# Kernel tuning notes

Measured on AMD Instinct MI355X. Metric: run time of the kernel, lower is better.

Reference implementation:

```python
import jax, jax.numpy as jnp
import numpy as np
from jax import lax


def setup_inputs() -> dict:
    key = jax.random.key(0)
    ks = jax.random.split(key, 6)
    B, S, C, HID, H, K = 8, 2048, 768, 768, 12, 9
    return {
        "query": jax.random.normal(ks[0], (B, S, C), jnp.float32),
        "value": jax.random.normal(ks[1], (B, S, C), jnp.float32),
        "hidden_states": jax.random.normal(ks[2], (B, S, HID), jnp.float32),
        "dw_weight": jax.random.normal(ks[3], (HID, 1, K), jnp.float32) * (2.0 / K) ** 0.5,
        "pw_weight": jax.random.normal(ks[4], (C, HID, 1), jnp.float32) * (2.0 / HID) ** 0.5,
        "sep_bias": jnp.zeros((C,), jnp.float32),
        "attn_W": jax.random.normal(ks[5], (H * K, C), jnp.float32) * (1.0 / C) ** 0.5,
        "attn_b": jnp.zeros((H * K,), jnp.float32),
        "num_heads": H,
        "kernel_size": K,
    }


def reference(query, value, hidden_states, dw_weight, pw_weight, sep_bias,
              attn_W, attn_b, num_heads, kernel_size):
    K = kernel_size
    H = num_heads
    B, S, C = value.shape  # all_head_size = C
    D = C // H             # attention_head_size
    HID = hidden_states.shape[-1]
    pad = K // 2

    # --- SeparableConv1d: depthwise (groups=HID) then pointwise 1x1 ---
    x = jnp.transpose(hidden_states, (0, 2, 1))  # [B, HID, S]
    dn = ("NCH", "OIH", "NCH")
    dw = lax.conv_general_dilated(x, dw_weight, window_strides=(1,),
                                  padding=[(pad, pad)], dimension_numbers=dn,
                                  feature_group_count=HID)  # [B, HID, S]
    pw = lax.conv_general_dilated(dw, pw_weight, window_strides=(1,),
                                  padding=[(0, 0)], dimension_numbers=dn)  # [B, C, S]
    ks_out = jnp.transpose(pw, (0, 2, 1)) + sep_bias  # [B, S, C]

    # --- dynamic conv kernel: gated projection + (double) softmax ---
    conv_attn = ks_out * query                                   # [B, S, C]
    filt = conv_attn @ attn_W.T + attn_b                          # [B, S, H*K]
    filt = filt.reshape(B, S, H, K)
    # original code applies softmax twice (once in SDConv, once in LightConv)
    filt = jax.nn.softmax(jax.nn.softmax(filt, axis=-1), axis=-1)

    # --- light conv: unfold value along seq and contract over window ---
    vpad = jnp.pad(value, ((0, 0), (pad, pad), (0, 0)))           # [B, S+K-1, C]
    unf = jnp.stack([vpad[:, k:k + S, :] for k in range(K)], axis=-1)  # [B,S,C,K]
    unf = unf.reshape(B, S, H, D, K)
    out = jnp.einsum("bshdk,bshk->bshd", unf, filt)               # [B,S,H,D]
    return out
```

## Files before the change

kernel.cpp:

```cpp
#include <hip/hip_runtime.h>
#include <hip/hip_bf16.h>
#include <stdint.h>

#define B_   8
#define S_   2048
#define C_   768
#define HID_ 768
#define H_   12
#define KW   9
#define D_   64
#define M_   (B_ * S_)
#define PADW 4
#define HK_  108
#define NPAD 128

typedef __attribute__((ext_vector_type(4))) float  floatx4;
typedef __attribute__((ext_vector_type(8))) __bf16 bf16x8;

#define GLD_LDS16(gptr, lptr)                                                  \
    __builtin_amdgcn_global_load_lds(                                          \
        (__attribute__((address_space(1))) void*)(gptr),                       \
        (__attribute__((address_space(3))) void*)(lptr), 16, 0, 0)

__global__ __launch_bounds__(256) void convert_w_kernel(
    const float* __restrict__ pwW, const float* __restrict__ attnW,
    __hip_bfloat16* __restrict__ pwWb, __hip_bfloat16* __restrict__ attnWb)
{
    int i = blockIdx.x * 256 + threadIdx.x;
    if (i < C_ * HID_) pwWb[i] = __float2bfloat16(pwW[i]);
    if (i < NPAD * HID_) {
        int n = i / HID_;
        float v = (n < HK_) ? attnW[i] : 0.0f;
        attnWb[i] = __float2bfloat16(v);
    }
}

#define TSD 16

__global__ __launch_bounds__(256) void dwconv_kernel(
    const float* __restrict__ hidden, const float* __restrict__ dw_w,
    __hip_bfloat16* __restrict__ dw_out)
{
    int idx  = blockIdx.x * 256 + threadIdx.x;
    int hq   = idx % (HID_ / 4);
    int rest = idx / (HID_ / 4);
    int sc   = rest % (S_ / TSD);
    int b    = rest / (S_ / TSD);
    int h    = hq * 4;
    int s0   = sc * TSD;
    size_t base = (size_t)b * S_ * HID_ + h;

    float w[36];
    const float4* wp = reinterpret_cast<const float4*>(dw_w + (size_t)h * KW);
#pragma unroll
    for (int i = 0; i < 9; ++i) {
        float4 t = wp[i];
        w[4 * i + 0] = t.x; w[4 * i + 1] = t.y;
        w[4 * i + 2] = t.z; w[4 * i + 3] = t.w;
    }

    float4 win[KW];
#pragma unroll
    for (int k = 0; k < 8; ++k) {
        int sp = s0 + k - PADW;
        float4 v = {0.f, 0.f, 0.f, 0.f};
        if ((unsigned)sp < (unsigned)S_)
            v = *reinterpret_cast<const float4*>(&hidden[base + (size_t)sp * HID_]);
        win[k] = v;
    }

#pragma unroll
    for (int i = 0; i < TSD; ++i) {
        int sp = s0 + i + PADW;
        float4 nv = {0.f, 0.f, 0.f, 0.f};
        if ((unsigned)sp < (unsigned)S_)
            nv = *reinterpret_cast<const float4*>(&hidden[base + (size_t)sp * HID_]);
        win[8] = nv;

        float a0 = 0.f, a1 = 0.f, a2 = 0.f, a3 = 0.f;
#pragma unroll
        for (int k = 0; k < KW; ++k) {
            a0 += win[k].x * w[k];
            a1 += win[k].y * w[9 + k];
            a2 += win[k].z * w[18 + k];
            a3 += win[k].w * w[27 + k];
        }
        union { __hip_bfloat16 bv[4]; uint2 u; } o;
        o.bv[0] = __float2bfloat16(a0);
        o.bv[1] = __float2bfloat16(a1);
        o.bv[2] = __float2bfloat16(a2);
        o.bv[3] = __float2bfloat16(a3);
        *reinterpret_cast<uint2*>(&dw_out[base + (size_t)(s0 + i) * HID_]) = o.u;

#pragma unroll
        for (int k = 0; k < 8; ++k) win[k] = win[k + 1];
    }
}

#define BKK 64

template <int MODE, int TBM>
__global__ __launch_bounds__(256) void gemm_bt_kernel(
    const __hip_bfloat16* __restrict__ A,
    const __hip_bfloat16* __restrict__ Bt,
    const float* __restrict__ bias,
    const float* __restrict__ query,
    __hip_bfloat16* __restrict__ outB,
    float* __restrict__ outF,
    int ntN)
{
    constexpr int MF = TBM / 32;
    __shared__ __align__(16) __hip_bfloat16 Alds[TBM * BKK];
    __shared__ __align__(16) __hip_bfloat16 Blds[64 * BKK];

    const int t    = threadIdx.x;
    const int lane = t & 63;
    const int wave = t >> 6;
    const int wr   = wave >> 1, wc = wave & 1;
    const int l16  = lane & 15, lq = lane >> 4;

    const int nwg  = (int)gridDim.x;
    const int chunk = nwg >> 3;
    const int wg   = ((int)blockIdx.x & 7) * chunk + ((int)blockIdx.x >> 3);

    const int tm   = wg / ntN;
    const int tn   = wg % ntN;
    const int row0 = tm * TBM;
    const int col0 = tn * 64;

    const int K = HID_;

    floatx4 acc[MF][2];
#pragma unroll
    for (int i = 0; i < MF; ++i)
#pragma unroll
        for (int j = 0; j < 2; ++j) acc[i][j] = (floatx4){0.f, 0.f, 0.f, 0.f};

    const int srow = t >> 3;
    const int scol = (t & 7) * 8;
    char* aBase = (char*)Alds + wave * 1024;
    char* bBase = (char*)Blds + wave * 1024;

    for (int kt = 0; kt < K; kt += BKK) {
#pragma unroll
        for (int i = 0; i < MF; ++i) {
            const __hip_bfloat16* ga = A + (size_t)(row0 + i * 32 + srow) * K + kt + scol;
            GLD_LDS16(const_cast<__hip_bfloat16*>(ga), aBase + i * 4096);
        }
#pragma unroll
        for (int i = 0; i < 2; ++i) {
            const __hip_bfloat16* gb = Bt + (size_t)(col0 + i * 32 + srow) * K + kt + scol;
            GLD_LDS16(const_cast<__hip_bfloat16*>(gb), bBase + i * 4096);
        }
        __syncthreads();

        const bf16x8* A8 = reinterpret_cast<const bf16x8*>(Alds);
        const bf16x8* B8 = reinterpret_cast<const bf16x8*>(Blds);
#pragma unroll
        for (int ks = 0; ks < 2; ++ks) {
            bf16x8 av[MF], bv[2];
#pragma unroll
            for (int m = 0; m < MF; ++m)
                av[m] = A8[(wr * (TBM / 2) + m * 16 + l16) * 8 + ks * 4 + lq];
#pragma unroll
            for (int n = 0; n < 2; ++n)
                bv[n] = B8[(wc * 32 + n * 16 + l16) * 8 + ks * 4 + lq];
#pragma unroll
            for (int m = 0; m < MF; ++m)
#pragma unroll
                for (int n = 0; n < 2; ++n)
                    acc[m][n] = __builtin_amdgcn_mfma_f32_16x16x32_bf16(
                        av[m], bv[n], acc[m][n], 0, 0, 0);
        }
        __syncthreads();
    }

    const int orow0 = row0 + wr * (TBM / 2);
    const int ocol0 = col0 + wc * 32;
#pragma unroll
    for (int m = 0; m < MF; ++m) {
#pragma unroll
        for (int n = 0; n < 2; ++n) {
            const int col = ocol0 + n * 16 + l16;
            if (MODE == 0) {
                const float bv = bias[col];
#pragma unroll
                for (int j = 0; j < 4; ++j) {
                    const int row = orow0 + m * 16 + lq * 4 + j;
                    float v = (acc[m][n][j] + bv) * query[(size_t)row * C_ + col];
                    outB[(size_t)row * C_ + col] = __float2bfloat16(v);
                }
            } else {
#pragma unroll
                for (int j = 0; j < 4; ++j) {
                    const int row = orow0 + m * 16 + lq * 4 + j;
                    outF[(size_t)row * NPAD + col] = acc[m][n][j];
                }
            }
        }
    }
}

__global__ __launch_bounds__(256) void softmax2_kernel(
    const float* __restrict__ logits, const float* __restrict__ attn_b,
    float* __restrict__ filt)
{
    int r = blockIdx.x * 256 + threadIdx.x;
    int h = r % H_;
    int m = r / H_;

    float v[KW];
#pragma unroll
    for (int k = 0; k < KW; ++k)
        v[k] = logits[(size_t)m * NPAD + h * KW + k] + attn_b[h * KW + k];

#pragma unroll
    for (int pass = 0; pass < 2; ++pass) {
        float mx = v[0];
#pragma unroll
        for (int k = 1; k < KW; ++k) mx = fmaxf(mx, v[k]);
        float s = 0.f;
#pragma unroll
        for (int k = 0; k < KW; ++k) { v[k] = __expf(v[k] - mx); s += v[k]; }
        float inv = 1.f / s;
#pragma unroll
        for (int k = 0; k < KW; ++k) v[k] *= inv;
    }
#pragma unroll
    for (int k = 0; k < KW; ++k) filt[(size_t)r * KW + k] = v[k];
}

#define TSL 16
#define SCHK 256

__global__ __launch_bounds__(256) void lightconv_kernel(
    const float* __restrict__ value, const float* __restrict__ filt,
    float* __restrict__ out)
{
    __shared__ float fl[SCHK * KW];

    const int tid = threadIdx.x;
    const int blk = blockIdx.x;
    const int nSC = S_ / SCHK;
    const int b   = blk / (H_ * nSC);
    const int rem = blk % (H_ * nSC);
    const int h   = rem / nSC;
    const int sch = rem % nSC;
    const int S0  = sch * SCHK;

    {
        const size_t r0 = ((size_t)b * S_ + S0) * H_ + h;
#pragma unroll
        for (int i = 0; i < 9; ++i) {
            int j  = tid + 256 * i;
            int so = j / KW;
            int k  = j - so * KW;
            fl[j] = filt[(r0 + (size_t)so * H_) * KW + k];
        }
    }
    __syncthreads();

    const int d4 = tid & 15;
    const int sg = tid >> 4;
    const int s0 = S0 + sg * TSL;
    const size_t vbase = (size_t)b * S_ * C_ + h * D_ + d4 * 4;
    const float* flrow = &fl[(sg * TSL) * KW];

    float4 win[KW];
#pragma unroll
    for (int k = 0; k < 8; ++k) {
        int sp = s0 + k - PADW;
        float4 v = {0.f, 0.f, 0.f, 0.f};
        if ((unsigned)sp < (unsigned)S_)
            v = *reinterpret_cast<const float4*>(&value[vbase + (size_t)sp * C_]);
        win[k] = v;
    }

#pragma unroll
    for (int i = 0; i < TSL; ++i) {
        int sp = s0 + i + PADW;
        float4 nv = {0.f, 0.f, 0.f, 0.f};
        if ((unsigned)sp < (unsigned)S_)
            nv = *reinterpret_cast<const float4*>(&value[vbase + (size_t)sp * C_]);
        win[8] = nv;

        float4 acc = {0.f, 0.f, 0.f, 0.f};
#pragma unroll
        for (int k = 0; k < KW; ++k) {
            float f = flrow[i * KW + k];
            acc.x += win[k].x * f;
            acc.y += win[k].y * f;
            acc.z += win[k].z * f;
            acc.w += win[k].w * f;
        }
        *reinterpret_cast<float4*>(&out[vbase + (size_t)(s0 + i) * C_]) = acc;

#pragma unroll
        for (int k = 0; k < 8; ++k) win[k] = win[k + 1];
    }
}

extern "C" void kernel_launch(void* const* d_in, const int* in_sizes, int n_in,
                              void* d_out, int out_size, void* d_ws, size_t ws_size,
                              hipStream_t stream)
{
    const float* query  = (const float*)d_in[0];
    const float* value  = (const float*)d_in[1];
    const float* hidden = (const float*)d_in[2];
    const float* dw_w   = (const float*)d_in[3];
    const float* pw_w   = (const float*)d_in[4];
    const float* sep_b  = (const float*)d_in[5];
    const float* attn_W = (const float*)d_in[6];
    const float* attn_b = (const float*)d_in[7];
    float* out = (float*)d_out;

    char* ws = (char*)d_ws;
    __hip_bfloat16* dwb    = (__hip_bfloat16*)(ws);
    __hip_bfloat16* cab    = (__hip_bfloat16*)(ws + 25165824);
    __hip_bfloat16* pwWb   = (__hip_bfloat16*)(ws + 50331648);
    __hip_bfloat16* attnWb = (__hip_bfloat16*)(ws + 51511296);
    float*          logits = (float*)(ws + 51707904);
    float*          filt   = (float*)(ws + 60096512);

    convert_w_kernel<<<(C_ * HID_) / 256, 256, 0, stream>>>(pw_w, attn_W, pwWb, attnWb);

    dwconv_kernel<<<(M_ * (HID_ / 4)) / (256 * TSD), 256, 0, stream>>>(hidden, dw_w, dwb);

    gemm_bt_kernel<0, 128><<<(M_ / 128) * (C_ / 64), 256, 0, stream>>>(
        dwb, pwWb, sep_b, query, cab, nullptr, C_ / 64);

    gemm_bt_kernel<1, 64><<<(M_ / 64) * (NPAD / 64), 256, 0, stream>>>(
        cab, attnWb, nullptr, nullptr, nullptr, logits, NPAD / 64);

    softmax2_kernel<<<(M_ * H_) / 256, 256, 0, stream>>>(logits, attn_b, filt);

    lightconv_kernel<<<B_ * H_ * (S_ / SCHK), 256, 0, stream>>>(value, filt, out);
}
```

Measured before the change: 106.6 us.

## Replace pointwise GEMM with 256x256 double-buffered 8-phase pipelined MFMA kernel

The pointwise-conv GEMM (16384x768x768) moves from a 128x64 tile kernel with a load-then-sync-then-compute loop to a 512-thread kernel with 256x256 tiles. It uses double-buffered LDS filled by global_load_lds, XOR-swizzled LDS addressing, and an 8-phase schedule that overlaps the next tile's loads with MFMA work on the current one. This is meant to raise data reuse, cut LDS bank conflicts and hide global memory latency. The cost is 128 KB of LDS per block and only 192 blocks, which may leave some compute units underused. It also relies on hand-placed vmcnt waits and barriers being correct.

```diff
diff --git a/kernel.cpp b/kernel.cpp
--- a/kernel.cpp
+++ b/kernel.cpp
@@ -22,6 +22,11 @@
         (__attribute__((address_space(1))) void*)(gptr),                       \
         (__attribute__((address_space(3))) void*)(lptr), 16, 0, 0)
 
+#define WAITVM4() do { asm volatile("s_waitcnt vmcnt(4)" ::: "memory"); \
+                       __builtin_amdgcn_sched_barrier(0); } while (0)
+#define WAITVM0() do { asm volatile("s_waitcnt vmcnt(0)" ::: "memory"); \
+                       __builtin_amdgcn_sched_barrier(0); } while (0)
+
 __global__ __launch_bounds__(256) void convert_w_kernel(
     const float* __restrict__ pwW, const float* __restrict__ attnW,
     __hip_bfloat16* __restrict__ pwWb, __hip_bfloat16* __restrict__ attnWb)
@@ -97,18 +102,143 @@
     }
 }
 
-#define BKK 64
-
-template <int MODE, int TBM>
-__global__ __launch_bounds__(256) void gemm_bt_kernel(
+__global__ __launch_bounds__(512, 2) void gemm1_8phase_kernel(
     const __hip_bfloat16* __restrict__ A,
     const __hip_bfloat16* __restrict__ Bt,
     const float* __restrict__ bias,
     const float* __restrict__ query,
-    __hip_bfloat16* __restrict__ outB,
+    __hip_bfloat16* __restrict__ outB)
+{
+    __shared__ __align__(16) __hip_bfloat16 Ash[2][2][128 * 64];
+    __shared__ __align__(16) __hip_bfloat16 Bsh[2][2][128 * 64];
+
+    const int t    = threadIdx.x;
+    const int lane = t & 63;
+    const int wave = t >> 6;
+    const int wr   = wave >> 2;
+    const int wc   = wave & 3;
+    const int l16  = lane & 15, lq = lane >> 4;
+
+    const int bid = (int)blockIdx.x;
+    const int wg  = (bid & 7) * 24 + (bid >> 3);
+    const int tm  = wg / 3, tn = wg % 3;
+    const int row0 = tm * 256, col0 = tn * 256;
+
+    const int srow    = wave * 8 + (lane >> 3);
+    const int srcslot = (lane & 7) ^ ((lane >> 3) & 7);
+    const __hip_bfloat16* aSrc = A  + (size_t)(row0 + srow) * HID_ + srcslot * 8;
+    const __hip_bfloat16* bSrc = Bt + (size_t)(col0 + srow) * HID_ + srcslot * 8;
+
+    floatx4 acc[2][2][4][2];
+#pragma unroll
+    for (int a = 0; a < 2; ++a)
+#pragma unroll
+    for (int b = 0; b < 2; ++b)
+#pragma unroll
+    for (int m = 0; m < 4; ++m)
+#pragma unroll
+    for (int n = 0; n < 2; ++n) acc[a][b][m][n] = (floatx4){0.f, 0.f, 0.f, 0.f};
+
+#define STG_A(tile, h) do {                                                    \
+    const __hip_bfloat16* _g = aSrc + (size_t)(h) * 128 * HID_ + (tile) * 64;  \
+    char* _l = (char*)(&Ash[(tile) & 1][h][0]) + wave * 1024;                  \
+    GLD_LDS16(_g, _l);                                                         \
+    GLD_LDS16(_g + 64 * HID_, _l + 8192);                                      \
+} while (0)
+
+#define STG_B(tile, h) do {                                                    \
+    const __hip_bfloat16* _g = bSrc + (size_t)(h) * 128 * HID_ + (tile) * 64;  \
+    char* _l = (char*)(&Bsh[(tile) & 1][h][0]) + wave * 1024;                  \
+    GLD_LDS16(_g, _l);                                                         \
+    GLD_LDS16(_g + 64 * HID_, _l + 8192);                                      \
+} while (0)
+
+#define PHASE(buf, mh, nh, STAGES, BOUNDARY) do {                              \
+    bf16x8 av[4][2], bv[2][2];                                                 \
+    const char* _ab = (const char*)(&Ash[buf][mh][0]);                         \
+    const char* _bb = (const char*)(&Bsh[buf][nh][0]);                         \
+    _Pragma("unroll") for (int _m = 0; _m < 4; ++_m) {                         \
+        const int _r = wr * 64 + _m * 16 + l16;                                \
+        _Pragma("unroll") for (int _k = 0; _k < 2; ++_k)                       \
+            av[_m][_k] = *(const bf16x8*)(_ab + _r * 128 +                     \
+                ((_k * 64 + lq * 16) ^ ((l16 & 7) << 4)));                     \
+    }                                                                          \
+    _Pragma("unroll") for (int _n = 0; _n < 2; ++_n) {                         \
+        const int _r = wc * 32 + _n * 16 + l16;                                \
+        _Pragma("unroll") for (int _k = 0; _k < 2; ++_k)                       \
+            bv[_n][_k] = *(const bf16x8*)(_bb + _r * 128 +                     \
+                ((_k * 64 + lq * 16) ^ ((l16 & 7) << 4)));                     \
+    }                                                                          \
+    STAGES;                                                                    \
+    __builtin_amdgcn_s_barrier();                                              \
+    asm volatile("s_waitcnt lgkmcnt(0)" ::: "memory");                         \
+    __builtin_amdgcn_sched_barrier(0);                                         \
+    __builtin_amdgcn_s_setprio(1);                                             \
+    _Pragma("unroll") for (int _m = 0; _m < 4; ++_m)                           \
+        _Pragma("unroll") for (int _n = 0; _n < 2; ++_n)                       \
+            _Pragma("unroll") for (int _k = 0; _k < 2; ++_k)                   \
+                acc[mh][nh][_m][_n] = __builtin_amdgcn_mfma_f32_16x16x32_bf16( \
+                    av[_m][_k], bv[_n][_k], acc[mh][nh][_m][_n], 0, 0, 0);     \
+    __builtin_amdgcn_s_setprio(0);                                             \
+    BOUNDARY;                                                                  \
+    __builtin_amdgcn_s_barrier();                                              \
+} while (0)
+
+    STG_A(0, 0);
+    STG_B(0, 1);
+    STG_B(0, 0);
+    STG_A(0, 1);
+    STG_A(1, 0);
+    STG_B(1, 1);
+    WAITVM4();
+    __builtin_amdgcn_s_barrier();
+
+    for (int it = 0; it < 6; ++it) {
+        const int t1 = 2 * it + 1, t2 = 2 * it + 2, t3 = 2 * it + 3;
+        const bool nl = (it < 5);
+        PHASE(0, 0, 0, { STG_B(t1, 0); }, {});
+        PHASE(0, 0, 1, { STG_A(t1, 1); }, {});
+        PHASE(0, 1, 1, { if (nl) STG_A(t2, 0); }, {});
+        PHASE(0, 1, 0, { if (nl) STG_B(t2, 1); },
+              { if (nl) { WAITVM4(); } else { WAITVM0(); } });
+        PHASE(1, 0, 0, { if (nl) STG_B(t2, 0); }, {});
+        PHASE(1, 0, 1, { if (nl) STG_A(t2, 1); }, {});
+        PHASE(1, 1, 1, { if (nl) STG_A(t3, 0); }, {});
+        PHASE(1, 1, 0, { if (nl) STG_B(t3, 1); }, { if (nl) WAITVM4(); });
+    }
+
+#pragma unroll
+    for (int mh = 0; mh < 2; ++mh)
+#pragma unroll
+    for (int nh = 0; nh < 2; ++nh)
+#pragma unroll
+    for (int n = 0; n < 2; ++n) {
+        const int col = col0 + nh * 128 + wc * 32 + n * 16 + l16;
+        const float bvv = bias[col];
+#pragma unroll
+        for (int m = 0; m < 4; ++m) {
+#pragma unroll
+            for (int j = 0; j < 4; ++j) {
+                const int row = row0 + mh * 128 + wr * 64 + m * 16 + lq * 4 + j;
+                float v = (acc[mh][nh][m][n][j] + bvv) * query[(size_t)row * C_ + col];
+                outB[(size_t)row * C_ + col] = __float2bfloat16(v);
+            }
+        }
+    }
+#undef STG_A
+#undef STG_B
+#undef PHASE
+}
+
+#define BKK 64
+
+__global__ __launch_bounds__(256) void gemm2_kernel(
+    const __hip_bfloat16* __restrict__ A,
+    const __hip_bfloat16* __restrict__ Bt,
     float* __restrict__ outF,
     int ntN)
 {
+    constexpr int TBM = 64;
     constexpr int MF = TBM / 32;
     __shared__ __align__(16) __hip_bfloat16 Alds[TBM * BKK];
     __shared__ __align__(16) __hip_bfloat16 Blds[64 * BKK];
@@ -145,12 +275,12 @@
 #pragma unroll
         for (int i = 0; i < MF; ++i) {
             const __hip_bfloat16* ga = A + (size_t)(row0 + i * 32 + srow) * K + kt + scol;
-            GLD_LDS16(const_cast<__hip_bfloat16*>(ga), aBase + i * 4096);
+            GLD_LDS16(ga, aBase + i * 4096);
         }
 #pragma unroll
         for (int i = 0; i < 2; ++i) {
             const __hip_bfloat16* gb = Bt + (size_t)(col0 + i * 32 + srow) * K + kt + scol;
-            GLD_LDS16(const_cast<__hip_bfloat16*>(gb), bBase + i * 4096);
+            GLD_LDS16(gb, bBase + i * 4096);
         }
         __syncthreads();
 
@@ -178,27 +308,16 @@
     const int orow0 = row0 + wr * (TBM / 2);
     const int ocol0 = col0 + wc * 32;
 #pragma unroll
-    for (int m = 0; m < MF; ++m) {
+    for (int m = 0; m < MF; ++m)
 #pragma unroll
         for (int n = 0; n < 2; ++n) {
             const int col = ocol0 + n * 16 + l16;
-            if (MODE == 0) {
-                const float bv = bias[col];
-#pragma unroll
-                for (int j = 0; j < 4; ++j) {
-                    const int row = orow0 + m * 16 + lq * 4 + j;
-                    float v = (acc[m][n][j] + bv) * query[(size_t)row * C_ + col];
-                    outB[(size_t)row * C_ + col] = __float2bfloat16(v);
-                }
-            } else {
-#pragma unroll
-                for (int j = 0; j < 4; ++j) {
-                    const int row = orow0 + m * 16 + lq * 4 + j;
-                    outF[(size_t)row * NPAD + col] = acc[m][n][j];
-                }
+#pragma unroll
+            for (int j = 0; j < 4; ++j) {
+                const int row = orow0 + m * 16 + lq * 4 + j;
+                outF[(size_t)row * NPAD + col] = acc[m][n][j];
             }
         }
-    }
 }
 
 __global__ __launch_bounds__(256) void softmax2_kernel(
@@ -326,11 +445,11 @@
 
     dwconv_kernel<<<(M_ * (HID_ / 4)) / (256 * TSD), 256, 0, stream>>>(hidden, dw_w, dwb);
 
-    gemm_bt_kernel<0, 128><<<(M_ / 128) * (C_ / 64), 256, 0, stream>>>(
-        dwb, pwWb, sep_b, query, cab, nullptr, C_ / 64);
-
-    gemm_bt_kernel<1, 64><<<(M_ / 64) * (NPAD / 64), 256, 0, stream>>>(
-        cab, attnWb, nullptr, nullptr, nullptr, logits, NPAD / 64);
+    gemm1_8phase_kernel<<<(M_ / 256) * (C_ / 256), 512, 0, stream>>>(
+        dwb, pwWb, sep_b, query, cab);
+
+    gemm2_kernel<<<(M_ / 64) * (NPAD / 64), 256, 0, stream>>>(
+        cab, attnWb, logits, NPAD / 64);
 
     softmax2_kernel<<<(M_ * H_) / 256, 256, 0, stream>>>(logits, attn_b, filt);
 
```

Result: slower. 112.7 us (+5.8%).

## Fuse pointwise GEMM, gating, attention projection and double softmax into one kernel

Applied to the files above, without the earlier changes.

Replaces the two GEMM launches and the softmax kernel with one kernel per 64-row block. The kernel computes the pointwise conv tile by tile over 128 output channels, applies bias and query gating, and stages the bf16 product in swizzled LDS. From there it accumulates the attention-logit GEMM directly, then runs the double softmax from LDS and writes only the filter. This removes the bf16 conv_attn and fp32 logits round trips through global memory and two launches. It adds double-buffered async LDS staging with XOR swizzle and explicit waitcnt/barriers. The trade-offs are fewer blocks (M/64), attn weights read from global inside the loop, and more intricate synchronisation.

```diff
diff --git a/kernel.cpp b/kernel.cpp
--- a/kernel.cpp
+++ b/kernel.cpp
@@ -22,6 +22,11 @@
         (__attribute__((address_space(1))) void*)(gptr),                       \
         (__attribute__((address_space(3))) void*)(lptr), 16, 0, 0)
 
+#define BARR() do { __builtin_amdgcn_s_barrier();                              \
+                    __builtin_amdgcn_sched_barrier(0); } while (0)
+#define LGKM0() do { asm volatile("s_waitcnt lgkmcnt(0)" ::: "memory");        \
+                     __builtin_amdgcn_sched_barrier(0); } while (0)
+
 __global__ __launch_bounds__(256) void convert_w_kernel(
     const float* __restrict__ pwW, const float* __restrict__ attnW,
     __hip_bfloat16* __restrict__ pwWb, __hip_bfloat16* __restrict__ attnWb)
@@ -97,137 +102,186 @@
     }
 }
 
-#define BKK 64
-
-template <int MODE, int TBM>
-__global__ __launch_bounds__(256) void gemm_bt_kernel(
+__global__ __launch_bounds__(512, 2) void fused_gemm_kernel(
     const __hip_bfloat16* __restrict__ A,
     const __hip_bfloat16* __restrict__ Bt,
+    const __hip_bfloat16* __restrict__ Wt,
     const float* __restrict__ bias,
     const float* __restrict__ query,
-    __hip_bfloat16* __restrict__ outB,
-    float* __restrict__ outF,
-    int ntN)
-{
-    constexpr int MF = TBM / 32;
-    __shared__ __align__(16) __hip_bfloat16 Alds[TBM * BKK];
-    __shared__ __align__(16) __hip_bfloat16 Blds[64 * BKK];
+    const float* __restrict__ attn_b,
+    float* __restrict__ filt)
+{
+    __shared__ __align__(16) char lds[49152];
+    char* Plds = lds;
+    float* LG  = (float*)(lds + 16384);
 
     const int t    = threadIdx.x;
     const int lane = t & 63;
     const int wave = t >> 6;
-    const int wr   = wave >> 1, wc = wave & 1;
+    const int wr   = wave >> 2;
+    const int wc   = wave & 3;
     const int l16  = lane & 15, lq = lane >> 4;
 
-    const int nwg  = (int)gridDim.x;
-    const int chunk = nwg >> 3;
-    const int wg   = ((int)blockIdx.x & 7) * chunk + ((int)blockIdx.x >> 3);
-
-    const int tm   = wg / ntN;
-    const int tn   = wg % ntN;
-    const int row0 = tm * TBM;
-    const int col0 = tn * 64;
-
-    const int K = HID_;
-
-    floatx4 acc[MF][2];
-#pragma unroll
-    for (int i = 0; i < MF; ++i)
-#pragma unroll
-        for (int j = 0; j < 2; ++j) acc[i][j] = (floatx4){0.f, 0.f, 0.f, 0.f};
-
-    const int srow = t >> 3;
-    const int scol = (t & 7) * 8;
-    char* aBase = (char*)Alds + wave * 1024;
-    char* bBase = (char*)Blds + wave * 1024;
-
-    for (int kt = 0; kt < K; kt += BKK) {
-#pragma unroll
-        for (int i = 0; i < MF; ++i) {
-            const __hip_bfloat16* ga = A + (size_t)(row0 + i * 32 + srow) * K + kt + scol;
-            GLD_LDS16(const_cast<__hip_bfloat16*>(ga), aBase + i * 4096);
-        }
-#pragma unroll
-        for (int i = 0; i < 2; ++i) {
-            const __hip_bfloat16* gb = Bt + (size_t)(col0 + i * 32 + srow) * K + kt + scol;
-            GLD_LDS16(const_cast<__hip_bfloat16*>(gb), bBase + i * 4096);
-        }
-        __syncthreads();
-
-        const bf16x8* A8 = reinterpret_cast<const bf16x8*>(Alds);
-        const bf16x8* B8 = reinterpret_cast<const bf16x8*>(Blds);
-#pragma unroll
-        for (int ks = 0; ks < 2; ++ks) {
-            bf16x8 av[MF], bv[2];
-#pragma unroll
-            for (int m = 0; m < MF; ++m)
-                av[m] = A8[(wr * (TBM / 2) + m * 16 + l16) * 8 + ks * 4 + lq];
-#pragma unroll
-            for (int n = 0; n < 2; ++n)
-                bv[n] = B8[(wc * 32 + n * 16 + l16) * 8 + ks * 4 + lq];
-#pragma unroll
-            for (int m = 0; m < MF; ++m)
+    const int row0 = (int)blockIdx.x * 64;
+
+    const int sr8     = lane >> 3;
+    const int srcslot = (lane & 7) ^ sr8;
+    const __hip_bfloat16* aS = A + (size_t)(row0 + wave * 8 + sr8) * HID_ + srcslot * 8;
+
+    floatx4 acc2[2][2];
+#pragma unroll
+    for (int m = 0; m < 2; ++m)
+#pragma unroll
+        for (int n = 0; n < 2; ++n) acc2[m][n] = (floatx4){0.f, 0.f, 0.f, 0.f};
+
+    for (int nt = 0; nt < 6; ++nt) {
+        const __hip_bfloat16* bS =
+            Bt + (size_t)(nt * 128 + wave * 8 + sr8) * HID_ + srcslot * 8;
+
+        floatx4 acc1[2][2];
+#pragma unroll
+        for (int m = 0; m < 2; ++m)
+#pragma unroll
+            for (int n = 0; n < 2; ++n) acc1[m][n] = (floatx4){0.f, 0.f, 0.f, 0.f};
+
+#define FSTG(kt, buf) do {                                                     \
+        GLD_LDS16(aS + (kt) * 64, lds + (buf) * 8192 + wave * 1024);           \
+        GLD_LDS16(bS + (kt) * 64, lds + 16384 + (buf) * 16384 + wave * 1024);  \
+        GLD_LDS16(bS + 64 * HID_ + (kt) * 64,                                  \
+                  lds + 16384 + (buf) * 16384 + 8192 + wave * 1024);           \
+    } while (0)
+
+        FSTG(0, 0);
+#pragma unroll 2
+        for (int kt = 0; kt < 12; ++kt) {
+            const int cur = kt & 1;
+            if (kt < 11) {
+                FSTG(kt + 1, cur ^ 1);
+                asm volatile("s_waitcnt vmcnt(3)" ::: "memory");
+            } else {
+                asm volatile("s_waitcnt vmcnt(0)" ::: "memory");
+            }
+            __builtin_amdgcn_sched_barrier(0);
+            BARR();
+
+            const char* ab = lds + cur * 8192;
+            const char* bb = lds + 16384 + cur * 16384;
+            bf16x8 av[2][2], bv[2][2];
+#pragma unroll
+            for (int m = 0; m < 2; ++m) {
+                const int r = wr * 32 + m * 16 + l16;
+#pragma unroll
+                for (int ks = 0; ks < 2; ++ks)
+                    av[m][ks] = *(const bf16x8*)(ab + r * 128 +
+                        ((ks * 64 + lq * 16) ^ ((l16 & 7) << 4)));
+            }
+#pragma unroll
+            for (int n = 0; n < 2; ++n) {
+                const int r = wc * 32 + n * 16 + l16;
+#pragma unroll
+                for (int ks = 0; ks < 2; ++ks)
+                    bv[n][ks] = *(const bf16x8*)(bb + r * 128 +
+                        ((ks * 64 + lq * 16) ^ ((l16 & 7) << 4)));
+            }
+            __builtin_amdgcn_s_setprio(1);
+#pragma unroll
+            for (int m = 0; m < 2; ++m)
 #pragma unroll
                 for (int n = 0; n < 2; ++n)
-                    acc[m][n] = __builtin_amdgcn_mfma_f32_16x16x32_bf16(
-                        av[m], bv[n], acc[m][n], 0, 0, 0);
-        }
-        __syncthreads();
-    }
-
-    const int orow0 = row0 + wr * (TBM / 2);
-    const int ocol0 = col0 + wc * 32;
-#pragma unroll
-    for (int m = 0; m < MF; ++m) {
+#pragma unroll
+                    for (int ks = 0; ks < 2; ++ks)
+                        acc1[m][n] = __builtin_amdgcn_mfma_f32_16x16x32_bf16(
+                            av[m][ks], bv[n][ks], acc1[m][n], 0, 0, 0);
+            __builtin_amdgcn_s_setprio(0);
+            LGKM0();
+            BARR();
+        }
+#undef FSTG
+
+#pragma unroll
+        for (int m = 0; m < 2; ++m)
+#pragma unroll
+            for (int n = 0; n < 2; ++n) {
+                const int cl   = wc * 32 + n * 16 + l16;
+                const int gcol = nt * 128 + cl;
+                const float bvv = bias[gcol];
+#pragma unroll
+                for (int j = 0; j < 4; ++j) {
+                    const int row = wr * 32 + m * 16 + lq * 4 + j;
+                    float v = (acc1[m][n][j] + bvv) *
+                              query[(size_t)(row0 + row) * C_ + gcol];
+                    __hip_bfloat16 hb = __float2bfloat16(v);
+                    *(uint16_t*)(Plds + row * 256 +
+                                 ((cl * 2) ^ ((row & 7) << 4))) =
+                        *(uint16_t*)&hb;
+                }
+            }
+        LGKM0();
+        BARR();
+
+#pragma unroll
+        for (int kk = 0; kk < 4; ++kk) {
+            bf16x8 pv[2], wv[2];
+#pragma unroll
+            for (int m = 0; m < 2; ++m) {
+                const int r = wr * 32 + m * 16 + l16;
+                pv[m] = *(const bf16x8*)(Plds + r * 256 +
+                    ((kk * 64 + lq * 16) ^ ((l16 & 7) << 4)));
+            }
+#pragma unroll
+            for (int n = 0; n < 2; ++n) {
+                const int wrow = wc * 32 + n * 16 + l16;
+                wv[n] = *(const bf16x8*)(Wt + (size_t)wrow * C_ +
+                                         nt * 128 + kk * 32 + lq * 8);
+            }
+#pragma unroll
+            for (int m = 0; m < 2; ++m)
+#pragma unroll
+                for (int n = 0; n < 2; ++n)
+                    acc2[m][n] = __builtin_amdgcn_mfma_f32_16x16x32_bf16(
+                        pv[m], wv[n], acc2[m][n], 0, 0, 0);
+        }
+        LGKM0();
+        BARR();
+    }
+
+#pragma unroll
+    for (int m = 0; m < 2; ++m)
 #pragma unroll
         for (int n = 0; n < 2; ++n) {
-            const int col = ocol0 + n * 16 + l16;
-            if (MODE == 0) {
-                const float bv = bias[col];
-#pragma unroll
-                for (int j = 0; j < 4; ++j) {
-                    const int row = orow0 + m * 16 + lq * 4 + j;
-                    float v = (acc[m][n][j] + bv) * query[(size_t)row * C_ + col];
-                    outB[(size_t)row * C_ + col] = __float2bfloat16(v);
-                }
-            } else {
-#pragma unroll
-                for (int j = 0; j < 4; ++j) {
-                    const int row = orow0 + m * 16 + lq * 4 + j;
-                    outF[(size_t)row * NPAD + col] = acc[m][n][j];
-                }
-            }
-        }
-    }
-}
-
-__global__ __launch_bounds__(256) void softmax2_kernel(
-    const float* __restrict__ logits, const float* __restrict__ attn_b,
-    float* __restrict__ filt)
-{
-    int r = blockIdx.x * 256 + threadIdx.x;
-    int h = r % H_;
-    int m = r / H_;
-
-    float v[KW];
-#pragma unroll
-    for (int k = 0; k < KW; ++k)
-        v[k] = logits[(size_t)m * NPAD + h * KW + k] + attn_b[h * KW + k];
-
-#pragma unroll
-    for (int pass = 0; pass < 2; ++pass) {
-        float mx = v[0];
-#pragma unroll
-        for (int k = 1; k < KW; ++k) mx = fmaxf(mx, v[k]);
-        float s = 0.f;
-#pragma unroll
-        for (int k = 0; k < KW; ++k) { v[k] = __expf(v[k] - mx); s += v[k]; }
-        float inv = 1.f / s;
-#pragma unroll
-        for (int k = 0; k < KW; ++k) v[k] *= inv;
-    }
-#pragma unroll
-    for (int k = 0; k < KW; ++k) filt[(size_t)r * KW + k] = v[k];
+            const int cl = wc * 32 + n * 16 + l16;
+#pragma unroll
+            for (int j = 0; j < 4; ++j) {
+                const int row = wr * 32 + m * 16 + lq * 4 + j;
+                LG[row * 128 + cl] = acc2[m][n][j];
+            }
+        }
+    LGKM0();
+    BARR();
+
+    for (int id = t; id < 64 * H_; id += 512) {
+        const int row = id / H_;
+        const int h   = id - row * H_;
+        float v[KW];
+#pragma unroll
+        for (int k = 0; k < KW; ++k)
+            v[k] = LG[row * 128 + h * KW + k] + attn_b[h * KW + k];
+#pragma unroll
+        for (int pass = 0; pass < 2; ++pass) {
+            float mx = v[0];
+#pragma unroll
+            for (int k = 1; k < KW; ++k) mx = fmaxf(mx, v[k]);
+            float s = 0.f;
+#pragma unroll
+            for (int k = 0; k < KW; ++k) { v[k] = __expf(v[k] - mx); s += v[k]; }
+            float inv = 1.f / s;
+#pragma unroll
+            for (int k = 0; k < KW; ++k) v[k] *= inv;
+        }
+        const size_t base = ((size_t)(row0 + row) * H_ + h) * KW;
+#pragma unroll
+        for (int k = 0; k < KW; ++k) filt[base + k] = v[k];
+    }
 }
 
 #define TSL 16
@@ -316,23 +370,16 @@
 
     char* ws = (char*)d_ws;
     __hip_bfloat16* dwb    = (__hip_bfloat16*)(ws);
-    __hip_bfloat16* cab    = (__hip_bfloat16*)(ws + 25165824);
-    __hip_bfloat16* pwWb   = (__hip_bfloat16*)(ws + 50331648);
-    __hip_bfloat16* attnWb = (__hip_bfloat16*)(ws + 51511296);
-    float*          logits = (float*)(ws + 51707904);
-    float*          filt   = (float*)(ws + 60096512);
+    __hip_bfloat16* pwWb   = (__hip_bfloat16*)(ws + 25165824);
+    __hip_bfloat16* attnWb = (__hip_bfloat16*)(ws + 26345472);
+    float*          filt   = (float*)(ws + 26542080);
 
     convert_w_kernel<<<(C_ * HID_) / 256, 256, 0, stream>>>(pw_w, attn_W, pwWb, attnWb);
 
     dwconv_kernel<<<(M_ * (HID_ / 4)) / (256 * TSD), 256, 0, stream>>>(hidden, dw_w, dwb);
 
-    gemm_bt_kernel<0, 128><<<(M_ / 128) * (C_ / 64), 256, 0, stream>>>(
-        dwb, pwWb, sep_b, query, cab, nullptr, C_ / 64);
-
-    gemm_bt_kernel<1, 64><<<(M_ / 64) * (NPAD / 64), 256, 0, stream>>>(
-        cab, attnWb, nullptr, nullptr, nullptr, logits, NPAD / 64);
-
-    softmax2_kernel<<<(M_ * H_) / 256, 256, 0, stream>>>(logits, attn_b, filt);
+    fused_gemm_kernel<<<M_ / 64, 512, 0, stream>>>(
+        dwb, pwWb, attnWb, sep_b, query, attn_b, filt);
 
     lightconv_kernel<<<B_ * H_ * (S_ / SCHK), 256, 0, stream>>>(value, filt, out);
 }
```

New measurement: 100.9 us. -5.3%, faster.
